# Performance work log

Measured on AMD Instinct MI355X. Metric: run time of the kernel, lower is better.

Reference implementation:

```python
import jax, jax.numpy as jnp
import numpy as np

# FlowNetC correlation hyperparameters (from init_kwargs)
PAD = 20
KS = 1
MD = 20
S1 = 1
S2 = 2
MUL = 1


def setup_inputs() -> dict:
    key = jax.random.key(0)
    k1, k2 = jax.random.split(key)
    B, C, H, W = 8, 256, 96, 128
    input1 = jax.random.normal(k1, (B, C, H, W), dtype=jnp.float32)
    input2 = jax.random.normal(k2, (B, C, H, W), dtype=jnp.float32)
    return {"input1": input1, "input2": input2}


def _correlation(in1, in2):
    b, c, h, w = in1.shape
    p1 = jnp.pad(in1, ((0, 0), (0, 0), (PAD, PAD), (PAD, PAD)))
    p2 = jnp.pad(in2, ((0, 0), (0, 0), (PAD, PAD), (PAD, PAD)))
    hp, wp = h + 2 * PAD, w + 2 * PAD
    out_h = (hp - 2 * MD - KS) // S1 + 1
    out_w = (wp - 2 * MD - KS) // S1 + 1
    d = 2 * MD // S2 + 1  # number of displacement steps per axis (21)

    # fixed center region of input1: [b, c, out_h, out_w]
    region1 = p1[:, :, MD:MD + out_h * S1:S1, MD:MD + out_w * S1:S1]

    offs = (jnp.arange(d) - d // 2) * S2  # displacement offsets
    dys, dxs = jnp.meshgrid(offs, offs, indexing='ij')
    dys = dys.reshape(-1)
    dxs = dxs.reshape(-1)

    def step(carry, dydx):
        dy, dx = dydx
        y0 = MD + dy
        x0 = MD + dx
        valid = (y0 >= 0) & (x0 >= 0) & (y0 + out_h * S1 <= hp) & (x0 + out_w * S1 <= wp)
        reg2 = jax.lax.dynamic_slice(
            p2, (0, 0, y0, x0), (b, c, out_h * S1, out_w * S1)
        )[:, :, ::S1, ::S1]
        corr = (region1 * reg2).sum(axis=1) * MUL  # [b, out_h, out_w]
        corr = jnp.where(valid, corr, jnp.zeros_like(corr))
        return carry, corr

    _, chans = jax.lax.scan(step, None, (dys, dxs))  # [d*d, b, out_h, out_w]
    return jnp.transpose(chans, (1, 0, 2, 3))  # [b, d*d, out_h, out_w]


def reference(input1, input2):
    return _correlation(input1, input2)
```

## Files before the change

### kernel.cpp

```cpp
#include <hip/hip_runtime.h>
#include <stdint.h>

#define B_N   8
#define C_N   256
#define H_N   96
#define W_N   128
#define KC    32
#define NCK   8
#define ND    21
#define NK    (ND * ND)

typedef __attribute__((ext_vector_type(8))) short short8;
typedef __attribute__((ext_vector_type(4))) float f32x4;

__device__ __forceinline__ uint32_t f2bf(float f) {
  uint32_t u = __builtin_bit_cast(uint32_t, f);
  return (u + 0x7fffu + ((u >> 16) & 1u)) >> 16;
}
__device__ __forceinline__ uint32_t packbf(float lo, float hi) {
  return f2bf(lo) | (f2bf(hi) << 16);
}
__device__ __forceinline__ void async16(void* lds_dst, const void* gsrc) {
  __builtin_amdgcn_global_load_lds(
      (const __attribute__((address_space(1))) void*)gsrc,
      (__attribute__((address_space(3))) void*)lds_dst, 16, 0, 0);
}

__global__ __launch_bounds__(256) void prep_a(const float* __restrict__ in1,
                                              unsigned short* __restrict__ Apre) {
  __shared__ float tile[KC][W_N + 1];
  int blk = blockIdx.x;
  int ck = blk & 7, bi = blk >> 3;
  int b = bi / H_N, i = bi % H_N;
  const float* src = in1 + ((size_t)(b * C_N + ck * KC) * H_N + i) * W_N;
  int tid = threadIdx.x;
  for (int idx = tid; idx < KC * W_N; idx += 256) {
    int c = idx >> 7, j = idx & 127;
    tile[c][j] = src[(size_t)c * (H_N * W_N) + j];
  }
  __syncthreads();
  uint32_t* dst = (uint32_t*)(Apre + ((size_t)blk << 12));
  for (int q = tid; q < 2048; q += 256) {
    int cm2 = q & 15, p = (q >> 4) & 1, je = q >> 5;
    int j = 2 * je + p;
    dst[q] = packbf(tile[2 * cm2][j], tile[2 * cm2 + 1][j]);
  }
}

__global__ __launch_bounds__(256) void prep_b(const float* __restrict__ in2,
                                              unsigned short* __restrict__ Bpre) {
  __shared__ float tile[KC][W_N + 1];
  int blk = blockIdx.x;
  int ck = blk & 7, bi = blk >> 3;
  int b = bi / H_N, y = bi % H_N;
  const float* src = in2 + ((size_t)(b * C_N + ck * KC) * H_N + y) * W_N;
  int tid = threadIdx.x;
  for (int idx = tid; idx < KC * W_N; idx += 256) {
    int c = idx >> 7, j = idx & 127;
    tile[c][j] = src[(size_t)c * (H_N * W_N) + j];
  }
  __syncthreads();
  uint32_t* dst = (uint32_t*)(Bpre + (size_t)blk * 6144);
  for (int q = tid; q < 3072; q += 256) {
    int cm2 = q & 15, p = (q >> 4) & 1, u = q >> 5;
    int x = 2 * u - 20 + p;
    uint32_t v = 0;
    if ((unsigned)x < 128u) v = packbf(tile[2 * cm2][x], tile[2 * cm2 + 1][x]);
    dst[q] = v;
  }
}

__global__ __launch_bounds__(256, 4) void corr_main(const unsigned short* __restrict__ Apre,
                                                    const unsigned short* __restrict__ Bpre,
                                                    float* __restrict__ out) {
  __shared__ __align__(16) char lds[45056];
  char* Xl = lds;
  char* Yl = lds + 8192;
  float* outl = (float*)(lds + 8192);

  int h = blockIdx.x;
  int l = (h & 7) * 672 + (h >> 3);
  int bi = l / 7, gidx = l - 7 * bi;
  int b = bi / H_N, i = bi % H_N;
  int dyb = gidx * 3;

  int tid = threadIdx.x;
  int lane = tid & 63, w = tid >> 6;
  int p = w & 1, th = w >> 1;
  int m = lane & 15, kg = lane >> 4;

  f32x4 acc[2][3][3];
#pragma unroll
  for (int a0 = 0; a0 < 2; ++a0)
#pragma unroll
    for (int a1 = 0; a1 < 3; ++a1)
#pragma unroll
      for (int a2 = 0; a2 < 3; ++a2) acc[a0][a1][a2] = {0.f, 0.f, 0.f, 0.f};

  uint32_t innsw = (uint32_t)(p * 64 + kg * 16) ^ ((uint32_t)(m & 7) << 4);

  for (int ck = 0; ck < NCK; ++ck) {
    __syncthreads();
    const char* Ab = (const char*)Apre + ((size_t)(bi * NCK + ck) << 13);
#pragma unroll
    for (int r = 0; r < 2; ++r) {
      uint32_t wb = (uint32_t)r * 4096u + (uint32_t)w * 1024u;
      uint32_t s = wb + (uint32_t)lane * 16u;
      uint32_t gb = s ^ (((s >> 7) & 7u) << 4);
      async16(Xl + wb, Ab + gb);
    }
#pragma unroll
    for (int q = 0; q < 9; ++q) {
      int L = w + q * 4;
      int g = L / 12, r12 = L - g * 12;
      int y = i + 2 * (dyb + g) - 20;
      char* lptr = Yl + L * 1024;
      if ((unsigned)y < (unsigned)H_N) {
        uint32_t s = (uint32_t)r12 * 1024u + (uint32_t)lane * 16u;
        uint32_t gb = s ^ (((s >> 7) & 7u) << 4);
        const char* Bb = (const char*)Bpre + (size_t)((b * H_N + y) * NCK + ck) * 12288;
        async16(lptr, Bb + gb);
      } else {
        short8 z = {};
        *(short8*)(lptr + lane * 16) = z;
      }
    }
    __syncthreads();
    short8 a0 = *(const short8*)(Xl + (16 * (2 * th + 0) + m) * 128 + innsw);
    short8 a1 = *(const short8*)(Xl + (16 * (2 * th + 1) + m) * 128 + innsw);
#pragma unroll
    for (int ss = 0; ss < 4; ++ss) {
      int s = 2 * th + ss;
      int u = 16 * s + m;
#pragma unroll
      for (int g = 0; g < 3; ++g) {
        short8 bb = *(const short8*)(Yl + g * 12288 + u * 128 + innsw);
        if (ss <= 2) acc[0][g][ss]     = __builtin_amdgcn_mfma_f32_16x16x32_bf16(a0, bb, acc[0][g][ss], 0, 0, 0);
        if (ss >= 1) acc[1][g][ss - 1] = __builtin_amdgcn_mfma_f32_16x16x32_bf16(a1, bb, acc[1][g][ss - 1], 0, 0, 0);
      }
    }
  }

#pragma unroll
  for (int g = 0; g < 3; ++g) {
    __syncthreads();
#pragma unroll
    for (int tt = 0; tt < 2; ++tt) {
      int t = 2 * th + tt;
#pragma unroll
      for (int dl = 0; dl < 3; ++dl) {
#pragma unroll
        for (int r = 0; r < 4; ++r) {
          int a_ = kg * 4 + r;
          int dxi = 16 * dl + m - a_;
          if (dxi >= 0 && dxi <= 20) {
            int j = 2 * (16 * t + a_) + p;
            outl[dxi * 129 + j] = acc[tt][g][dl][r];
          }
        }
      }
    }
    __syncthreads();
    int dyi = dyb + g;
    size_t obase = ((size_t)(b * NK + dyi * ND) * H_N + i) * W_N;
    for (int idx = tid; idx < ND * W_N; idx += 256) {
      int dxi = idx >> 7, j = idx & 127;
      out[obase + (size_t)dxi * (H_N * W_N) + j] = outl[dxi * 129 + j];
    }
  }
}

__global__ void corr_naive(const float* __restrict__ in1, const float* __restrict__ in2,
                           float* __restrict__ out) {
  size_t o = (size_t)blockIdx.x * 256 + threadIdx.x;
  const size_t total = (size_t)B_N * NK * H_N * W_N;
  if (o >= total) return;
  int j = o & 127;
  int i = (int)((o >> 7) % H_N);
  int k = (int)((o / ((size_t)H_N * W_N)) % NK);
  int b = (int)(o / ((size_t)NK * H_N * W_N));
  int dyi = k / ND, dxi = k % ND;
  int y = i + 2 * dyi - 20, x = j + 2 * dxi - 20;
  float s = 0.f;
  if ((unsigned)y < (unsigned)H_N && (unsigned)x < (unsigned)W_N) {
    const float* p1 = in1 + ((size_t)b * C_N * H_N + i) * W_N + j;
    const float* p2 = in2 + ((size_t)b * C_N * H_N + y) * W_N + x;
    for (int c = 0; c < C_N; ++c)
      s += p1[(size_t)c * H_N * W_N] * p2[(size_t)c * H_N * W_N];
  }
  out[o] = s;
}

extern "C" void kernel_launch(void* const* d_in, const int* in_sizes, int n_in,
                              void* d_out, int out_size, void* d_ws, size_t ws_size,
                              hipStream_t stream) {
  const float* in1 = (const float*)d_in[0];
  const float* in2 = (const float*)d_in[1];
  float* out = (float*)d_out;

  const size_t A_BYTES = (size_t)B_N * H_N * NCK * 64 * 64 * 2;
  const size_t B_BYTES = (size_t)B_N * H_N * NCK * 96 * 64 * 2;
  if (ws_size < A_BYTES + B_BYTES) {
    size_t total = (size_t)B_N * NK * H_N * W_N;
    corr_naive<<<(int)((total + 255) / 256), 256, 0, stream>>>(in1, in2, out);
    return;
  }
  unsigned short* Apre = (unsigned short*)d_ws;
  unsigned short* Bpre = (unsigned short*)((char*)d_ws + A_BYTES);

  prep_a<<<B_N * H_N * NCK, 256, 0, stream>>>(in1, Apre);
  prep_b<<<B_N * H_N * NCK, 256, 0, stream>>>(in2, Bpre);
  corr_main<<<5376, 256, 0, stream>>>(Apre, Bpre, out);
}
```

Measured before the change: 207.4 us.

## Pre-swizzle operands into MFMA fragment layout and load directly from global

The prep stage now writes A and B in per-lane MFMA fragment order, so corr_main reads its operands straight from global memory into registers instead of staging them through LDS with async copies and barriers. Out-of-range B rows point at a zero buffer with zero stride. The two prep kernels are merged into one launch, and occupancy bounds are relaxed to 3 waves to allow more registers for the preloaded B fragments. This removes the LDS staging and per-chunk synchronisation, but each block now fetches from global or L2 on every K chunk with less explicit reuse.

```diff
diff --git a/kernel.cpp b/kernel.cpp
--- a/kernel.cpp
+++ b/kernel.cpp
@@ -5,13 +5,14 @@
 #define C_N   256
 #define H_N   96
 #define W_N   128
-#define KC    32
 #define NCK   8
 #define ND    21
 #define NK    (ND * ND)
 
 typedef __attribute__((ext_vector_type(8))) short short8;
 typedef __attribute__((ext_vector_type(4))) float f32x4;
+
+__device__ char zchunk[12288];
 
 __device__ __forceinline__ uint32_t f2bf(float f) {
   uint32_t u = __builtin_bit_cast(uint32_t, f);
@@ -20,63 +21,51 @@
 __device__ __forceinline__ uint32_t packbf(float lo, float hi) {
   return f2bf(lo) | (f2bf(hi) << 16);
 }
-__device__ __forceinline__ void async16(void* lds_dst, const void* gsrc) {
-  __builtin_amdgcn_global_load_lds(
-      (const __attribute__((address_space(1))) void*)gsrc,
-      (__attribute__((address_space(3))) void*)lds_dst, 16, 0, 0);
-}
 
-__global__ __launch_bounds__(256) void prep_a(const float* __restrict__ in1,
-                                              unsigned short* __restrict__ Apre) {
-  __shared__ float tile[KC][W_N + 1];
+__global__ __launch_bounds__(256) void prep(const float* __restrict__ in1,
+                                            const float* __restrict__ in2,
+                                            unsigned short* __restrict__ Apre,
+                                            unsigned short* __restrict__ Bpre) {
+  __shared__ float tile[32][W_N + 1];
   int blk = blockIdx.x;
-  int ck = blk & 7, bi = blk >> 3;
-  int b = bi / H_N, i = bi % H_N;
-  const float* src = in1 + ((size_t)(b * C_N + ck * KC) * H_N + i) * W_N;
+  bool isA = blk < 6144;
+  int rblk = isA ? blk : blk - 6144;
+  int ck = rblk & 7, bi = rblk >> 3;
+  int b = bi / H_N, row = bi % H_N;
+  const float* src = (isA ? in1 : in2) + ((size_t)(b * C_N + ck * 32) * H_N + row) * W_N;
   int tid = threadIdx.x;
-  for (int idx = tid; idx < KC * W_N; idx += 256) {
+  for (int idx = tid; idx < 32 * W_N; idx += 256) {
     int c = idx >> 7, j = idx & 127;
     tile[c][j] = src[(size_t)c * (H_N * W_N) + j];
   }
   __syncthreads();
-  uint32_t* dst = (uint32_t*)(Apre + ((size_t)blk << 12));
-  for (int q = tid; q < 2048; q += 256) {
-    int cm2 = q & 15, p = (q >> 4) & 1, je = q >> 5;
-    int j = 2 * je + p;
-    dst[q] = packbf(tile[2 * cm2][j], tile[2 * cm2 + 1][j]);
+  if (isA) {
+    uint32_t* dst = (uint32_t*)Apre + (size_t)rblk * 2048;
+    for (int q = tid; q < 2048; q += 256) {
+      int e2 = q & 3, ln = (q >> 2) & 63, tp = q >> 8;
+      int t = tp >> 1, p = tp & 1;
+      int m = ln & 15, kg = ln >> 4;
+      int c0 = kg * 8 + 2 * e2;
+      int j = 32 * t + 2 * m + p;
+      dst[q] = packbf(tile[c0][j], tile[c0 + 1][j]);
+    }
+  } else {
+    uint32_t* dst = (uint32_t*)Bpre + (size_t)rblk * 3072;
+    for (int q = tid; q < 3072; q += 256) {
+      int e2 = q & 3, ln = (q >> 2) & 63, sp = q >> 8;
+      int s = sp >> 1, p = sp & 1;
+      int m = ln & 15, kg = ln >> 4;
+      int c0 = kg * 8 + 2 * e2;
+      int x = 32 * s + 2 * m - 20 + p;
+      dst[q] = ((unsigned)x < 128u) ? packbf(tile[c0][x], tile[c0 + 1][x]) : 0u;
+    }
   }
 }
 
-__global__ __launch_bounds__(256) void prep_b(const float* __restrict__ in2,
-                                              unsigned short* __restrict__ Bpre) {
-  __shared__ float tile[KC][W_N + 1];
-  int blk = blockIdx.x;
-  int ck = blk & 7, bi = blk >> 3;
-  int b = bi / H_N, y = bi % H_N;
-  const float* src = in2 + ((size_t)(b * C_N + ck * KC) * H_N + y) * W_N;
-  int tid = threadIdx.x;
-  for (int idx = tid; idx < KC * W_N; idx += 256) {
-    int c = idx >> 7, j = idx & 127;
-    tile[c][j] = src[(size_t)c * (H_N * W_N) + j];
-  }
-  __syncthreads();
-  uint32_t* dst = (uint32_t*)(Bpre + (size_t)blk * 6144);
-  for (int q = tid; q < 3072; q += 256) {
-    int cm2 = q & 15, p = (q >> 4) & 1, u = q >> 5;
-    int x = 2 * u - 20 + p;
-    uint32_t v = 0;
-    if ((unsigned)x < 128u) v = packbf(tile[2 * cm2][x], tile[2 * cm2 + 1][x]);
-    dst[q] = v;
-  }
-}
-
-__global__ __launch_bounds__(256, 4) void corr_main(const unsigned short* __restrict__ Apre,
+__global__ __launch_bounds__(256, 3) void corr_main(const unsigned short* __restrict__ Apre,
                                                     const unsigned short* __restrict__ Bpre,
                                                     float* __restrict__ out) {
-  __shared__ __align__(16) char lds[45056];
-  char* Xl = lds;
-  char* Yl = lds + 8192;
-  float* outl = (float*)(lds + 8192);
+  __shared__ float outl[ND][W_N + 1];
 
   int h = blockIdx.x;
   int l = (h & 7) * 672 + (h >> 3);
@@ -91,54 +80,45 @@
 
   f32x4 acc[2][3][3];
 #pragma unroll
-  for (int a0 = 0; a0 < 2; ++a0)
+  for (int a0i = 0; a0i < 2; ++a0i)
 #pragma unroll
-    for (int a1 = 0; a1 < 3; ++a1)
+    for (int a1i = 0; a1i < 3; ++a1i)
 #pragma unroll
-      for (int a2 = 0; a2 < 3; ++a2) acc[a0][a1][a2] = {0.f, 0.f, 0.f, 0.f};
+      for (int a2i = 0; a2i < 3; ++a2i) acc[a0i][a1i][a2i] = {0.f, 0.f, 0.f, 0.f};
 
-  uint32_t innsw = (uint32_t)(p * 64 + kg * 16) ^ ((uint32_t)(m & 7) << 4);
+  const char* Ap = (const char*)Apre + (size_t)bi * 65536
+                   + (((4 * th + p)) << 10) + lane * 16;
+  const char* Bp[3];
+  int bstr[3];
+#pragma unroll
+  for (int g = 0; g < 3; ++g) {
+    int y = i + 2 * (dyb + g) - 20;
+    bool v = (unsigned)y < (unsigned)H_N;
+    const char* base = v ? (const char*)Bpre + (size_t)(b * H_N + y) * 98304
+                         : (const char*)zchunk;
+    Bp[g] = base + ((4 * th + p) << 10) + lane * 16;
+    bstr[g] = v ? 12288 : 0;
+  }
 
+#pragma unroll 2
   for (int ck = 0; ck < NCK; ++ck) {
-    __syncthreads();
-    const char* Ab = (const char*)Apre + ((size_t)(bi * NCK + ck) << 13);
+    short8 a0 = *(const short8*)(Ap);
+    short8 a1 = *(const short8*)(Ap + 2048);
+    short8 bb[4][3];
 #pragma unroll
-    for (int r = 0; r < 2; ++r) {
-      uint32_t wb = (uint32_t)r * 4096u + (uint32_t)w * 1024u;
-      uint32_t s = wb + (uint32_t)lane * 16u;
-      uint32_t gb = s ^ (((s >> 7) & 7u) << 4);
-      async16(Xl + wb, Ab + gb);
-    }
+    for (int ss = 0; ss < 4; ++ss)
 #pragma unroll
-    for (int q = 0; q < 9; ++q) {
-      int L = w + q * 4;
-      int g = L / 12, r12 = L - g * 12;
-      int y = i + 2 * (dyb + g) - 20;
-      char* lptr = Yl + L * 1024;
-      if ((unsigned)y < (unsigned)H_N) {
-        uint32_t s = (uint32_t)r12 * 1024u + (uint32_t)lane * 16u;
-        uint32_t gb = s ^ (((s >> 7) & 7u) << 4);
-        const char* Bb = (const char*)Bpre + (size_t)((b * H_N + y) * NCK + ck) * 12288;
-        async16(lptr, Bb + gb);
-      } else {
-        short8 z = {};
-        *(short8*)(lptr + lane * 16) = z;
-      }
-    }
-    __syncthreads();
-    short8 a0 = *(const short8*)(Xl + (16 * (2 * th + 0) + m) * 128 + innsw);
-    short8 a1 = *(const short8*)(Xl + (16 * (2 * th + 1) + m) * 128 + innsw);
+      for (int g = 0; g < 3; ++g)
+        bb[ss][g] = *(const short8*)(Bp[g] + ss * 2048);
 #pragma unroll
-    for (int ss = 0; ss < 4; ++ss) {
-      int s = 2 * th + ss;
-      int u = 16 * s + m;
+    for (int ss = 0; ss < 4; ++ss)
 #pragma unroll
       for (int g = 0; g < 3; ++g) {
-        short8 bb = *(const short8*)(Yl + g * 12288 + u * 128 + innsw);
-        if (ss <= 2) acc[0][g][ss]     = __builtin_amdgcn_mfma_f32_16x16x32_bf16(a0, bb, acc[0][g][ss], 0, 0, 0);
-        if (ss >= 1) acc[1][g][ss - 1] = __builtin_amdgcn_mfma_f32_16x16x32_bf16(a1, bb, acc[1][g][ss - 1], 0, 0, 0);
+        if (ss <= 2) acc[0][g][ss]     = __builtin_amdgcn_mfma_f32_16x16x32_bf16(a0, bb[ss][g], acc[0][g][ss], 0, 0, 0);
+        if (ss >= 1) acc[1][g][ss - 1] = __builtin_amdgcn_mfma_f32_16x16x32_bf16(a1, bb[ss][g], acc[1][g][ss - 1], 0, 0, 0);
       }
-    }
+    Ap += 8192;
+    Bp[0] += bstr[0]; Bp[1] += bstr[1]; Bp[2] += bstr[2];
   }
 
 #pragma unroll
@@ -155,7 +135,7 @@
           int dxi = 16 * dl + m - a_;
           if (dxi >= 0 && dxi <= 20) {
             int j = 2 * (16 * t + a_) + p;
-            outl[dxi * 129 + j] = acc[tt][g][dl][r];
+            outl[dxi][j] = acc[tt][g][dl][r];
           }
         }
       }
@@ -165,7 +145,7 @@
     size_t obase = ((size_t)(b * NK + dyi * ND) * H_N + i) * W_N;
     for (int idx = tid; idx < ND * W_N; idx += 256) {
       int dxi = idx >> 7, j = idx & 127;
-      out[obase + (size_t)dxi * (H_N * W_N) + j] = outl[dxi * 129 + j];
+      out[obase + (size_t)dxi * (H_N * W_N) + j] = outl[dxi][j];
     }
   }
 }
@@ -198,8 +178,8 @@
   const float* in2 = (const float*)d_in[1];
   float* out = (float*)d_out;
 
-  const size_t A_BYTES = (size_t)B_N * H_N * NCK * 64 * 64 * 2;
-  const size_t B_BYTES = (size_t)B_N * H_N * NCK * 96 * 64 * 2;
+  const size_t A_BYTES = (size_t)6144 * 8192;
+  const size_t B_BYTES = (size_t)6144 * 12288;
   if (ws_size < A_BYTES + B_BYTES) {
     size_t total = (size_t)B_N * NK * H_N * W_N;
     corr_naive<<<(int)((total + 255) / 256), 256, 0, stream>>>(in1, in2, out);
@@ -208,7 +188,6 @@
   unsigned short* Apre = (unsigned short*)d_ws;
   unsigned short* Bpre = (unsigned short*)((char*)d_ws + A_BYTES);
 
-  prep_a<<<B_N * H_N * NCK, 256, 0, stream>>>(in1, Apre);
-  prep_b<<<B_N * H_N * NCK, 256, 0, stream>>>(in2, Bpre);
+  prep<<<12288, 256, 0, stream>>>(in1, in2, Apre, Bpre);
   corr_main<<<5376, 256, 0, stream>>>(Apre, Bpre, out);
 }
```

Measured after the change: 213.2 us. 1.03x slower.
